# Kernel tuning notes

Measured on AMD Instinct MI355X. Metric: run time of the kernel, lower is better.

The kernel has to match this reference:

```python
import jax, jax.numpy as jnp
import numpy as np

T, HID, HQ, HKV, D = 2048, 4096, 32, 8, 128
ROPE_BASE = 10000.0


def setup_inputs() -> dict:
    key = jax.random.key(0)
    ks = jax.random.split(key, 5)
    scale = 0.02
    hidden_states = jax.random.normal(ks[0], (T, HID), dtype=jnp.float32)
    position_ids = jnp.arange(T, dtype=jnp.int32)
    # HF-style rotary tables: freqs duplicated along last dim -> [T, D]
    inv_freq = 1.0 / (ROPE_BASE ** (jnp.arange(0, D, 2, dtype=jnp.float32) / D))
    ang = position_ids.astype(jnp.float32)[:, None] * inv_freq[None, :]  # [T, D/2]
    emb = jnp.concatenate([ang, ang], axis=-1)  # [T, D]
    cos, sin = jnp.cos(emb), jnp.sin(emb)
    Wq = jax.random.normal(ks[1], (HID, HQ * D), dtype=jnp.float32) * scale
    Wk = jax.random.normal(ks[2], (HID, HKV * D), dtype=jnp.float32) * scale
    Wv = jax.random.normal(ks[3], (HID, HKV * D), dtype=jnp.float32) * scale
    Wo = jax.random.normal(ks[4], (HQ * D, HID), dtype=jnp.float32) * scale
    return {"hidden_states": hidden_states, "position_ids": position_ids,
            "cos": cos, "sin": sin, "Wq": Wq, "Wk": Wk, "Wv": Wv, "Wo": Wo}


def _rotate_half(x):
    x1, x2 = jnp.split(x, 2, axis=-1)
    return jnp.concatenate([-x2, x1], axis=-1)


def reference(hidden_states, position_ids, cos, sin, Wq, Wk, Wv, Wo):
    t = hidden_states.shape[0]
    scaling = D ** -0.5
    # QKV projections (attention_bias=False)
    q = (hidden_states @ Wq).reshape(t, HQ, D)   # [T, Hq, D]
    k = (hidden_states @ Wk).reshape(t, HKV, D)  # [T, Hkv, D]
    v = (hidden_states @ Wv).reshape(t, HKV, D)
    # RoPE: cos/sin [T, D] broadcast over heads
    c, s = cos[:, None, :], sin[:, None, :]
    q = q * c + _rotate_half(q) * s
    k = k * c + _rotate_half(k) * s
    # GQA: expand KV heads to query heads
    groups = HQ // HKV
    k = jnp.repeat(k, groups, axis=1)  # [T, Hq, D]
    v = jnp.repeat(v, groups, axis=1)
    # Causal attention
    scores = jnp.einsum('thd,shd->hts', q, k) * scaling  # [Hq, T, T]
    causal = jnp.tril(jnp.ones((t, t), dtype=bool))
    scores = jnp.where(causal[None], scores, jnp.finfo(scores.dtype).min)
    probs = jax.nn.softmax(scores, axis=-1)
    attn = jnp.einsum('hts,shd->thd', probs, v).reshape(t, HQ * D)
    return attn @ Wo
```

## Files before the change

kernel.cpp:

```cpp
#include <hip/hip_runtime.h>
#include <hip/hip_bf16.h>
#include <cstdint>
#include <cstddef>

#define T_DIM   2048
#define HID     4096
#define HQ      32
#define HKV     8
#define D_HEAD  128
#define QKV_N   6144
#define KOFF    4096
#define VOFF    5120

typedef __attribute__((ext_vector_type(8))) short short8;
typedef __attribute__((ext_vector_type(4))) float floatx4;

__device__ __forceinline__ ushort f2bf(float f) {
    union { float f; uint u; } v; v.f = f;
    uint r = v.u + 0x7fffu + ((v.u >> 16) & 1u);
    return (ushort)(r >> 16);
}
__device__ __forceinline__ float bf2f(ushort h) {
    union { uint u; float f; } v; v.u = ((uint)h) << 16; return v.f;
}
__device__ __forceinline__ short8 ld8(const ushort* p) {
    uint2 a = *(const uint2*)p, b = *(const uint2*)(p + 4);
    union { uint u[4]; short8 s; } x;
    x.u[0] = a.x; x.u[1] = a.y; x.u[2] = b.x; x.u[3] = b.y;
    return x.s;
}
__device__ __forceinline__ void gld_lds16(const ushort* g, ushort* l) {
    __builtin_amdgcn_global_load_lds(
        (__attribute__((address_space(1))) void*)(g),
        (__attribute__((address_space(3))) void*)(l), 16, 0, 0);
}

__global__ void cast_f32_bf16(const float* __restrict__ in, ushort* __restrict__ out, int n) {
    int i = (blockIdx.x * blockDim.x + threadIdx.x) * 4;
    if (i < n) {
        float4 v = *(const float4*)(in + i);
        ushort4 o;
        o.x = f2bf(v.x); o.y = f2bf(v.y); o.z = f2bf(v.z); o.w = f2bf(v.w);
        *(ushort4*)(out + i) = o;
    }
}

__global__ __launch_bounds__(256) void transpose_cast(const float* __restrict__ W,
                                                      ushort* __restrict__ Wt, int K, int N) {
    __shared__ ushort tile[64][66];
    int n0 = blockIdx.x * 64, k0 = blockIdx.y * 64;
    int tx = threadIdx.x & 15, ty = threadIdx.x >> 4;
#pragma unroll
    for (int i = 0; i < 4; i++) {
        int r = ty + i * 16;
        float4 v = *(const float4*)&W[(size_t)(k0 + r) * N + n0 + tx * 4];
        tile[tx * 4 + 0][r] = f2bf(v.x);
        tile[tx * 4 + 1][r] = f2bf(v.y);
        tile[tx * 4 + 2][r] = f2bf(v.z);
        tile[tx * 4 + 3][r] = f2bf(v.w);
    }
    __syncthreads();
#pragma unroll
    for (int i = 0; i < 4; i++) {
        int nr = ty + i * 16;
        ushort4 o = *(const ushort4*)&tile[nr][tx * 4];
        *(ushort4*)&Wt[(size_t)(n0 + nr) * K + k0 + tx * 4] = o;
    }
}

__global__ void transpose_v(const ushort* __restrict__ qkv, ushort* __restrict__ VtG) {
    __shared__ ushort tile[32][33];
    int t0 = blockIdx.x * 32, d0 = blockIdx.y * 32, kvh = blockIdx.z;
    int tx = threadIdx.x & 31, ty = threadIdx.x >> 5;
#pragma unroll
    for (int i = 0; i < 4; i++) {
        int t = t0 + ty + i * 8;
        tile[ty + i * 8][tx] = qkv[(size_t)t * QKV_N + VOFF + kvh * D_HEAD + d0 + tx];
    }
    __syncthreads();
#pragma unroll
    for (int i = 0; i < 4; i++) {
        int d = d0 + ty + i * 8;
        VtG[((size_t)kvh * D_HEAD + d) * T_DIM + t0 + tx] = tile[tx][ty + i * 8];
    }
}

template <typename OutT>
__global__ __launch_bounds__(256) void gemm_bt(const ushort* __restrict__ A,
                                               const ushort* __restrict__ Bt,
                                               OutT* __restrict__ C,
                                               int K, int lda, int ldb, int ldc) {
    __shared__ ushort As[128 * 32];
    __shared__ ushort Bs[128 * 32];
    int tid = threadIdx.x;
    int w = tid >> 6, lane = tid & 63, quad = lane >> 4, l15 = lane & 15;
    int wr = (w >> 1) * 64, wc = (w & 1) * 64;
    int m0 = blockIdx.y * 128, n0 = blockIdx.x * 128;

    floatx4 acc[4][4];
    floatx4 z = {0.f, 0.f, 0.f, 0.f};
#pragma unroll
    for (int i = 0; i < 4; i++)
#pragma unroll
        for (int j = 0; j < 4; j++) acc[i][j] = z;

    int arow = tid >> 2, ac = (tid & 3) * 8;
    const ushort* gA0 = A + (size_t)(m0 + arow) * lda + ac;
    const ushort* gA1 = A + (size_t)(m0 + arow + 64) * lda + ac;
    const ushort* gB0 = Bt + (size_t)(n0 + arow) * ldb + ac;
    const ushort* gB1 = Bt + (size_t)(n0 + arow + 64) * ldb + ac;

    for (int k0 = 0; k0 < K; k0 += 32) {
        __syncthreads();
        gld_lds16(gA0, &As[tid * 8]);
        gld_lds16(gA1, &As[64 * 32 + tid * 8]);
        gld_lds16(gB0, &Bs[tid * 8]);
        gld_lds16(gB1, &Bs[64 * 32 + tid * 8]);
        gA0 += 32; gA1 += 32; gB0 += 32; gB1 += 32;
        __syncthreads();

        short8 af[4];
#pragma unroll
        for (int i = 0; i < 4; i++)
            af[i] = *(const short8*)&As[(wr + i * 16 + l15) * 32 + quad * 8];
#pragma unroll
        for (int j = 0; j < 4; j++) {
            short8 bf = *(const short8*)&Bs[(wc + j * 16 + l15) * 32 + quad * 8];
#pragma unroll
            for (int i = 0; i < 4; i++)
                acc[i][j] = __builtin_amdgcn_mfma_f32_16x16x32_bf16(af[i], bf, acc[i][j], 0, 0, 0);
        }
    }

#pragma unroll
    for (int i = 0; i < 4; i++) {
        int row0 = m0 + wr + i * 16 + quad * 4;
#pragma unroll
        for (int j = 0; j < 4; j++) {
            int col = n0 + wc + j * 16 + l15;
#pragma unroll
            for (int r = 0; r < 4; r++) {
                float v = acc[i][j][r];
                if constexpr (sizeof(OutT) == 2)
                    C[(size_t)(row0 + r) * ldc + col] = (OutT)f2bf(v);
                else
                    C[(size_t)(row0 + r) * ldc + col] = v;
            }
        }
    }
}

__global__ void rope_kernel(ushort* __restrict__ qkv, const float* __restrict__ cosb,
                            const float* __restrict__ sinb) {
    int t = blockIdx.x;
    ushort* row = qkv + (size_t)t * QKV_N;
    const float* cr = cosb + (size_t)t * D_HEAD;
    const float* sr = sinb + (size_t)t * D_HEAD;
    for (int c = threadIdx.x; c < 2560; c += 256) {
        int slice = c >> 6, d = c & 63;
        int col = slice * 128 + d;
        float x0 = bf2f(row[col]), x1 = bf2f(row[col + 64]);
        float cs = cr[d], sn = sr[d];
        row[col] = f2bf(x0 * cs - x1 * sn);
        row[col + 64] = f2bf(x1 * cs + x0 * sn);
    }
}

#define PS_STRIDE 68

__global__ __launch_bounds__(256, 2) void attn_kernel(const ushort* __restrict__ qkv,
                                                      const ushort* __restrict__ VtG,
                                                      ushort* __restrict__ attn) {
    __shared__ ushort Ks[64 * 128];
    __shared__ ushort Vt[128 * 64];
    __shared__ ushort Ps[128 * PS_STRIDE];

    int qt = (gridDim.x - 1) - blockIdx.x;
    int h = blockIdx.y;
    int q0 = qt * 128;
    int kbmax = 2 * qt + 1;
    int tid = threadIdx.x, w = tid >> 6, lane = tid & 63, quad = lane >> 4, l15 = lane & 15;
    int kvh = h >> 2;

    const ushort* kbase = qkv + (size_t)KOFF + (size_t)kvh * D_HEAD;
    const ushort* vbase = VtG + (size_t)kvh * D_HEAD * T_DIM;

    const ushort* ksrc[4];
    const ushort* vsrc[4];
#pragma unroll
    for (int i = 0; i < 4; i++) {
        int cid = i * 256 + tid;
        int kr = cid >> 4, kp = cid & 15, kc = kp ^ (kr & 15);
        ksrc[i] = kbase + (size_t)kr * QKV_N + kc * 8;
        int vr = cid >> 3, vp = cid & 7, vc = vp ^ (vr & 7);
        vsrc[i] = vbase + (size_t)vr * T_DIM + vc * 8;
    }

    short8 qf[2][4];
#pragma unroll
    for (int s = 0; s < 2; s++) {
        const ushort* qrow = qkv + (size_t)(q0 + s * 64 + w * 16 + l15) * QKV_N + h * D_HEAD + quad * 8;
#pragma unroll
        for (int ks = 0; ks < 4; ks++)
            qf[s][ks] = *(const short8*)(qrow + ks * 32);
    }

    floatx4 o[2][8];
    floatx4 z = {0.f, 0.f, 0.f, 0.f};
#pragma unroll
    for (int s = 0; s < 2; s++)
#pragma unroll
        for (int j = 0; j < 8; j++) o[s][j] = z;
    float lsum[2][4] = {{0.f, 0.f, 0.f, 0.f}, {0.f, 0.f, 0.f, 0.f}};

    const float scale_l2e = 0.08838834764831845f * 1.4426950408889634f;
    const float BOUND = 24.0f;

    for (int kb = 0; kb <= kbmax; kb++) {
        bool act0 = (kb <= 2 * qt);

        __syncthreads();
#pragma unroll
        for (int i = 0; i < 4; i++) {
            gld_lds16(ksrc[i], &Ks[(i * 256 + tid) * 8]);
            gld_lds16(vsrc[i], &Vt[(i * 256 + tid) * 8]);
            ksrc[i] += (size_t)64 * QKV_N;
            vsrc[i] += 64;
        }
        __syncthreads();

        floatx4 sc[2][4];
#pragma unroll
        for (int s = 0; s < 2; s++)
#pragma unroll
            for (int jt = 0; jt < 4; jt++) sc[s][jt] = z;
#pragma unroll
        for (int ks = 0; ks < 4; ks++) {
#pragma unroll
            for (int jt = 0; jt < 4; jt++) {
                short8 kf = ld8(&Ks[(jt * 16 + l15) * 128 + (((ks * 4 + quad) ^ l15) * 8)]);
                if (act0)
                    sc[0][jt] = __builtin_amdgcn_mfma_f32_16x16x32_bf16(qf[0][ks], kf, sc[0][jt], 0, 0, 0);
                sc[1][jt] = __builtin_amdgcn_mfma_f32_16x16x32_bf16(qf[1][ks], kf, sc[1][jt], 0, 0, 0);
            }
        }

#pragma unroll
        for (int s = 0; s < 2; s++) {
            if (s == 0 && !act0) continue;
            bool diag = (kb == 2 * qt + s);
#pragma unroll
            for (int r = 0; r < 4; r++) {
                int rloc = w * 16 + quad * 4 + r;
#pragma unroll
                for (int jt = 0; jt < 4; jt++) {
                    float v = fmaf(sc[s][jt][r], scale_l2e, -BOUND);
                    if (diag && (jt * 16 + l15 > rloc)) v = -1e30f;
                    float p = exp2f(v);
                    lsum[s][r] += p;
                    Ps[(s * 64 + rloc) * PS_STRIDE + jt * 16 + l15] = f2bf(p);
                }
            }
        }

#pragma unroll
        for (int ks2 = 0; ks2 < 2; ks2++) {
            short8 pf0 = ld8(&Ps[(w * 16 + l15) * PS_STRIDE + ks2 * 32 + quad * 8]);
            short8 pf1 = ld8(&Ps[(64 + w * 16 + l15) * PS_STRIDE + ks2 * 32 + quad * 8]);
#pragma unroll
            for (int jt = 0; jt < 8; jt++) {
                short8 vf = ld8(&Vt[(jt * 16 + l15) * 64 + (((ks2 * 4 + quad) ^ (l15 & 7)) * 8)]);
                if (act0)
                    o[0][jt] = __builtin_amdgcn_mfma_f32_16x16x32_bf16(pf0, vf, o[0][jt], 0, 0, 0);
                o[1][jt] = __builtin_amdgcn_mfma_f32_16x16x32_bf16(pf1, vf, o[1][jt], 0, 0, 0);
            }
        }
    }

#pragma unroll
    for (int s = 0; s < 2; s++) {
#pragma unroll
        for (int r = 0; r < 4; r++) {
            float l = lsum[s][r];
#pragma unroll
            for (int mk = 1; mk <= 8; mk <<= 1) l += __shfl_xor(l, mk);
            float inv = 1.f / l;
            int trow = q0 + s * 64 + w * 16 + quad * 4 + r;
            ushort* orow = attn + (size_t)trow * (HQ * D_HEAD) + h * D_HEAD;
#pragma unroll
            for (int jt = 0; jt < 8; jt++)
                orow[jt * 16 + l15] = f2bf(o[s][jt][r] * inv);
        }
    }
}

extern "C" void kernel_launch(void* const* d_in, const int* in_sizes, int n_in,
                              void* d_out, int out_size, void* d_ws, size_t ws_size,
                              hipStream_t stream) {
    const float* hidden = (const float*)d_in[0];
    const float* cosb = (const float*)d_in[2];
    const float* sinb = (const float*)d_in[3];
    const float* Wq = (const float*)d_in[4];
    const float* Wk = (const float*)d_in[5];
    const float* Wv = (const float*)d_in[6];
    const float* Wo = (const float*)d_in[7];
    float* out = (float*)d_out;

    char* ws = (char*)d_ws;
    ushort* hiddenB = (ushort*)(ws);
    ushort* WqkvT   = (ushort*)(ws + (size_t)(16u << 20));
    ushort* WoT     = (ushort*)(ws + (size_t)(64u << 20));
    ushort* qkv     = (ushort*)(ws + (size_t)(96u << 20));
    ushort* attnO   = (ushort*)(ws + (size_t)(120u << 20));
    ushort* VtG     = (ushort*)(ws + (size_t)(136u << 20));

    cast_f32_bf16<<<8192, 256, 0, stream>>>(hidden, hiddenB, T_DIM * HID);
    transpose_cast<<<dim3(64, 64), 256, 0, stream>>>(Wq, WqkvT, HID, 4096);
    transpose_cast<<<dim3(16, 64), 256, 0, stream>>>(Wk, WqkvT + (size_t)4096 * HID, HID, 1024);
    transpose_cast<<<dim3(16, 64), 256, 0, stream>>>(Wv, WqkvT + (size_t)5120 * HID, HID, 1024);
    transpose_cast<<<dim3(64, 64), 256, 0, stream>>>(Wo, WoT, HID, 4096);

    gemm_bt<ushort><<<dim3(48, 16), 256, 0, stream>>>(hiddenB, WqkvT, qkv,
                                                      HID, HID, HID, QKV_N);
    rope_kernel<<<T_DIM, 256, 0, stream>>>(qkv, cosb, sinb);
    transpose_v<<<dim3(64, 4, 8), 256, 0, stream>>>(qkv, VtG);
    attn_kernel<<<dim3(T_DIM / 128, HQ), 256, 0, stream>>>(qkv, VtG, attnO);
    gemm_bt<float><<<dim3(32, 16), 256, 0, stream>>>(attnO, WoT, out,
                                                     HID, HID, HID, HID);
}
```

Measured before the change: 558.4 us.

## Double-buffer GEMM LDS tiles, overlap attention K loads, swap GEMM grid order

The GEMM kernel now keeps two LDS buffers for A and B. It prefetches the next K-slice while the MFMA runs on the current one, which removes one barrier per iteration. The attention kernel loads the first K tile before its loop and prefetches the next K tile during the P·V phase, with the barriers reordered to match. The GEMM launch grids are also transposed so consecutive blocks walk along M, which changes L2 reuse of the weight tiles. The cost is double the GEMM LDS usage, which may reduce occupancy, and correctness now relies on the barriers waiting for the async global-to-LDS loads.

```diff
diff --git a/kernel.cpp b/kernel.cpp
--- a/kernel.cpp
+++ b/kernel.cpp
@@ -90,12 +90,12 @@
                                                const ushort* __restrict__ Bt,
                                                OutT* __restrict__ C,
                                                int K, int lda, int ldb, int ldc) {
-    __shared__ ushort As[128 * 32];
-    __shared__ ushort Bs[128 * 32];
+    __shared__ ushort As[2][128 * 32];
+    __shared__ ushort Bs[2][128 * 32];
     int tid = threadIdx.x;
     int w = tid >> 6, lane = tid & 63, quad = lane >> 4, l15 = lane & 15;
     int wr = (w >> 1) * 64, wc = (w & 1) * 64;
-    int m0 = blockIdx.y * 128, n0 = blockIdx.x * 128;
+    int m0 = blockIdx.x * 128, n0 = blockIdx.y * 128;
 
     floatx4 acc[4][4];
     floatx4 z = {0.f, 0.f, 0.f, 0.f};
@@ -110,22 +110,30 @@
     const ushort* gB0 = Bt + (size_t)(n0 + arow) * ldb + ac;
     const ushort* gB1 = Bt + (size_t)(n0 + arow + 64) * ldb + ac;
 
-    for (int k0 = 0; k0 < K; k0 += 32) {
+    gld_lds16(gA0, &As[0][tid * 8]);
+    gld_lds16(gA1, &As[0][64 * 32 + tid * 8]);
+    gld_lds16(gB0, &Bs[0][tid * 8]);
+    gld_lds16(gB1, &Bs[0][64 * 32 + tid * 8]);
+    gA0 += 32; gA1 += 32; gB0 += 32; gB1 += 32;
+
+    int cur = 0;
+    for (int k0 = 0; k0 < K; k0 += 32, cur ^= 1) {
         __syncthreads();
-        gld_lds16(gA0, &As[tid * 8]);
-        gld_lds16(gA1, &As[64 * 32 + tid * 8]);
-        gld_lds16(gB0, &Bs[tid * 8]);
-        gld_lds16(gB1, &Bs[64 * 32 + tid * 8]);
-        gA0 += 32; gA1 += 32; gB0 += 32; gB1 += 32;
-        __syncthreads();
+        if (k0 + 32 < K) {
+            gld_lds16(gA0, &As[cur ^ 1][tid * 8]);
+            gld_lds16(gA1, &As[cur ^ 1][64 * 32 + tid * 8]);
+            gld_lds16(gB0, &Bs[cur ^ 1][tid * 8]);
+            gld_lds16(gB1, &Bs[cur ^ 1][64 * 32 + tid * 8]);
+            gA0 += 32; gA1 += 32; gB0 += 32; gB1 += 32;
+        }
 
         short8 af[4];
 #pragma unroll
         for (int i = 0; i < 4; i++)
-            af[i] = *(const short8*)&As[(wr + i * 16 + l15) * 32 + quad * 8];
+            af[i] = *(const short8*)&As[cur][(wr + i * 16 + l15) * 32 + quad * 8];
 #pragma unroll
         for (int j = 0; j < 4; j++) {
-            short8 bf = *(const short8*)&Bs[(wc + j * 16 + l15) * 32 + quad * 8];
+            short8 bf = *(const short8*)&Bs[cur][(wc + j * 16 + l15) * 32 + quad * 8];
 #pragma unroll
             for (int i = 0; i < 4; i++)
                 acc[i][j] = __builtin_amdgcn_mfma_f32_16x16x32_bf16(af[i], bf, acc[i][j], 0, 0, 0);
@@ -196,6 +204,12 @@
         vsrc[i] = vbase + (size_t)vr * T_DIM + vc * 8;
     }
 
+#pragma unroll
+    for (int i = 0; i < 4; i++) {
+        gld_lds16(ksrc[i], &Ks[(i * 256 + tid) * 8]);
+        ksrc[i] += (size_t)64 * QKV_N;
+    }
+
     short8 qf[2][4];
 #pragma unroll
     for (int s = 0; s < 2; s++) {
@@ -216,18 +230,16 @@
     const float scale_l2e = 0.08838834764831845f * 1.4426950408889634f;
     const float BOUND = 24.0f;
 
+    __syncthreads();
+
     for (int kb = 0; kb <= kbmax; kb++) {
         bool act0 = (kb <= 2 * qt);
 
-        __syncthreads();
 #pragma unroll
         for (int i = 0; i < 4; i++) {
-            gld_lds16(ksrc[i], &Ks[(i * 256 + tid) * 8]);
             gld_lds16(vsrc[i], &Vt[(i * 256 + tid) * 8]);
-            ksrc[i] += (size_t)64 * QKV_N;
             vsrc[i] += 64;
         }
-        __syncthreads();
 
         floatx4 sc[2][4];
 #pragma unroll
@@ -263,6 +275,16 @@
             }
         }
 
+        __syncthreads();
+
+        if (kb < kbmax) {
+#pragma unroll
+            for (int i = 0; i < 4; i++) {
+                gld_lds16(ksrc[i], &Ks[(i * 256 + tid) * 8]);
+                ksrc[i] += (size_t)64 * QKV_N;
+            }
+        }
+
 #pragma unroll
         for (int ks2 = 0; ks2 < 2; ks2++) {
             short8 pf0 = ld8(&Ps[(w * 16 + l15) * PS_STRIDE + ks2 * 32 + quad * 8]);
@@ -275,6 +297,8 @@
                 o[1][jt] = __builtin_amdgcn_mfma_f32_16x16x32_bf16(pf1, vf, o[1][jt], 0, 0, 0);
             }
         }
+
+        __syncthreads();
     }
 
 #pragma unroll
@@ -320,11 +344,11 @@
     transpose_cast<<<dim3(16, 64), 256, 0, stream>>>(Wv, WqkvT + (size_t)5120 * HID, HID, 1024);
     transpose_cast<<<dim3(64, 64), 256, 0, stream>>>(Wo, WoT, HID, 4096);
 
-    gemm_bt<ushort><<<dim3(48, 16), 256, 0, stream>>>(hiddenB, WqkvT, qkv,
+    gemm_bt<ushort><<<dim3(16, 48), 256, 0, stream>>>(hiddenB, WqkvT, qkv,
                                                       HID, HID, HID, QKV_N);
     rope_kernel<<<T_DIM, 256, 0, stream>>>(qkv, cosb, sinb);
     transpose_v<<<dim3(64, 4, 8), 256, 0, stream>>>(qkv, VtG);
     attn_kernel<<<dim3(T_DIM / 128, HQ), 256, 0, stream>>>(qkv, VtG, attnO);
-    gemm_bt<float><<<dim3(32, 16), 256, 0, stream>>>(attnO, WoT, out,
+    gemm_bt<float><<<dim3(16, 32), 256, 0, stream>>>(attnO, WoT, out,
                                                      HID, HID, HID, HID);
 }
```

Measured after the change: 540.3 us. 3.2% less time.
